# Performance work log

Hardware: AMD Instinct MI355X
Metric: run time of the kernel (lower is better)

## Reference

```python
import jax, jax.numpy as jnp
import numpy as np

B, N, C = 8, 16384, 256

def setup_inputs() -> dict:
    key = jax.random.key(0)
    ks = jax.random.split(key, 5)
    scale = 1.0 / np.sqrt(C)
    return {
        "x_in": jax.random.normal(ks[0], (B, N, C), dtype=jnp.float32),
        "Wq": jax.random.normal(ks[1], (C, C), dtype=jnp.float32) * scale,
        "bq": jax.random.normal(ks[2], (C,), dtype=jnp.float32) * scale,
        "Wk": jax.random.normal(ks[3], (C, C), dtype=jnp.float32) * scale,
        "bk": jax.random.normal(ks[4], (C,), dtype=jnp.float32) * scale,
    }

def reference(x_in, Wq, bq, Wk, bk):
    b, n, c = x_in.shape
    # Faithful to torch: reshape (NOT transpose) to [B, C, N]
    x = x_in.reshape(b, c, n)
    # 1x1 Conv1d == per-position linear over channel dim
    Q = jnp.einsum('oc,bcn->bon', Wq, x) + bq[None, :, None]  # [B,C,N]
    K = jnp.einsum('oc,bcn->bon', Wk, x) + bk[None, :, None]  # [B,C,N]
    # Q @ K^T over length axis -> channel-channel scores [B,C,C]
    scores = jnp.einsum('bcn,bdn->bcd', Q, K)
    c_c = jax.nn.softmax(scores, axis=-1)
    # x_in @ c_c + residual -> [B,N,C]
    return jnp.einsum('bnc,bcd->bnd', x_in, c_c) + x_in
```

## Files before the change

### kernel.cpp

```cpp
#include <hip/hip_runtime.h>

#define Bn 8
#define Nn 16384
#define Cn 256
#define NC 32

typedef __attribute__((ext_vector_type(4)))  float f32x4;
typedef __attribute__((ext_vector_type(16))) float f32x16;
typedef __attribute__((ext_vector_type(8)))  _Float16 f16x8;
typedef __attribute__((ext_vector_type(8)))  unsigned short u16x8;

static __device__ __forceinline__ unsigned short f2h(float f) {
    return __builtin_bit_cast(unsigned short, (_Float16)f);
}
static __device__ __forceinline__ f32x16 mfma16h(u16x8 a, u16x8 b, f32x16 c) {
    return __builtin_amdgcn_mfma_f32_32x32x16_f16(
        __builtin_bit_cast(f16x8, a), __builtin_bit_cast(f16x8, b), c, 0, 0, 0);
}

__global__ __launch_bounds__(256, 2) void k_gram(
    const float* __restrict__ x, float* __restrict__ gpart,
    float* __restrict__ spart) {
  const int b    = blockIdx.x & 7;
  const int loc  = blockIdx.x >> 3;
  const int ck   = loc >> 1;
  const int half = loc & 1;

  __shared__ __align__(16) char smem[2][32768];

  const int t     = threadIdx.x;
  const int lane  = t & 63;
  const int w     = t >> 6;
  const int ln    = lane & 31, kh = lane >> 5;
  const int rquad = t >> 4;
  const int c4    = t & 15;

  const float* xb = x + (size_t)b * ((size_t)Cn * Nn) + (size_t)ck * 512;

  f32x16 acc[4][2];
#pragma unroll
  for (int m = 0; m < 4; ++m)
#pragma unroll
    for (int n = 0; n < 2; ++n)
#pragma unroll
      for (int i = 0; i < 16; ++i) acc[m][n][i] = 0.f;

  float srow[16];
#pragma unroll
  for (int p = 0; p < 16; ++p) srow[p] = 0.f;

  f32x4 ldA[8], ldB[8];
#define LOADA(s) { _Pragma("unroll") for (int p = 0; p < 8; ++p) \
    ldA[p] = *(const f32x4*)(xb + (size_t)(p * 16 + rquad) * Nn + (s) * 64 + c4 * 4); }
#define LOADB(s) { _Pragma("unroll") for (int p = 0; p < 8; ++p) \
    ldB[p] = *(const f32x4*)(xb + (size_t)((p + 8) * 16 + rquad) * Nn + (s) * 64 + c4 * 4); }

  LOADA(0); LOADB(0);

  for (int s = 0; s < 8; ++s) {
    char* buf = smem[s & 1];
    __syncthreads();
#pragma unroll
    for (int p = 0; p < 8; ++p) {
      f32x4 v = ldA[p];
      srow[p] += (v.x + v.y) + (v.z + v.w);
      int r = p * 16 + rquad;
      ushort4 hv = make_ushort4(f2h(v.x), f2h(v.y), f2h(v.z), f2h(v.w));
      *(ushort4*)(buf + r * 128 + ((((c4 >> 1) + r) & 7) << 4) + (c4 & 1) * 8) = hv;
    }
#pragma unroll
    for (int p = 0; p < 8; ++p) {
      f32x4 v = ldB[p];
      srow[p + 8] += (v.x + v.y) + (v.z + v.w);
      int r = (p + 8) * 16 + rquad;
      ushort4 hv = make_ushort4(f2h(v.x), f2h(v.y), f2h(v.z), f2h(v.w));
      *(ushort4*)(buf + r * 128 + ((((c4 >> 1) + r) & 7) << 4) + (c4 & 1) * 8) = hv;
    }
    __syncthreads();
    if (s < 7) { LOADA(s + 1); LOADB(s + 1); }
#pragma unroll
    for (int ks = 0; ks < 4; ++ks) {
      const int cp = ks * 2 + kh;
      u16x8 A[4], Bv[2];
#pragma unroll
      for (int m = 0; m < 4; ++m) {
        int r = half * 128 + m * 32 + ln;
        A[m] = *(const u16x8*)(buf + r * 128 + (((cp + r) & 7) << 4));
      }
#pragma unroll
      for (int n = 0; n < 2; ++n) {
        int r = w * 64 + n * 32 + ln;
        Bv[n] = *(const u16x8*)(buf + r * 128 + (((cp + r) & 7) << 4));
      }
#pragma unroll
      for (int m = 0; m < 4; ++m)
#pragma unroll
        for (int n = 0; n < 2; ++n)
          acc[m][n] = mfma16h(A[m], Bv[n], acc[m][n]);
    }
  }
#undef LOADA
#undef LOADB

  if (half == 0) {
#pragma unroll
    for (int p = 0; p < 16; ++p) {
      float v = srow[p];
      v += __shfl_xor(v, 1);
      v += __shfl_xor(v, 2);
      v += __shfl_xor(v, 4);
      v += __shfl_xor(v, 8);
      if (c4 == 0) spart[(size_t)(b * NC + ck) * Cn + p * 16 + rquad] = v;
    }
  }

  float* gp = gpart + (size_t)(b * NC + ck) * (Cn * Cn);
#pragma unroll
  for (int m = 0; m < 4; ++m)
#pragma unroll
    for (int n = 0; n < 2; ++n)
#pragma unroll
      for (int r2 = 0; r2 < 16; ++r2) {
        int row = half * 128 + m * 32 + (r2 & 3) + 8 * (r2 >> 2) + 4 * kh;
        int col = w * 64 + n * 32 + ln;
        gp[row * Cn + col] = acc[m][n][r2];
      }
}

__global__ __launch_bounds__(256) void k_misc(
    const float* __restrict__ spart, const float* __restrict__ wk,
    const float* __restrict__ bk, float* __restrict__ sv,
    float* __restrict__ wkT, float* __restrict__ kN) {
  const int bb = blockIdx.x, t = threadIdx.x;
  __shared__ float s_l[256];
  float a = 0.f;
#pragma unroll
  for (int q = 0; q < NC; ++q) a += spart[(size_t)(bb * NC + q) * Cn + t];
  sv[bb * Cn + t] = a;
  s_l[t] = a;
#pragma unroll
  for (int j = 0; j < 32; ++j) {
    int k = bb * 32 + j;
    wkT[k * Cn + t] = wk[t * Cn + k];
  }
  __syncthreads();
  float k2 = 0.f;
  for (int c = 0; c < 256; ++c) k2 += wk[t * Cn + c] * s_l[c];
  kN[bb * Cn + t] = k2 + 16384.f * bk[t];
}

__global__ __launch_bounds__(256) void k_gk(
    const float* __restrict__ gpart, const float* __restrict__ sv,
    const float* __restrict__ wkT, const float* __restrict__ bk,
    float* __restrict__ GK) {
  const int b = blockIdx.x >> 6, tile = blockIdx.x & 63;
  const int r0 = tile * 4, t = threadIdx.x;
  __shared__ float g_l[4][256];

  float a[4] = {0.f, 0.f, 0.f, 0.f};
  const float* gp = gpart + (size_t)b * NC * 65536 + r0 * 256 + t;
  for (int ck = 0; ck < NC; ++ck) {
#pragma unroll
    for (int j = 0; j < 4; ++j) a[j] += gp[(size_t)ck * 65536 + j * 256];
  }
#pragma unroll
  for (int j = 0; j < 4; ++j) g_l[j][t] = a[j];
  __syncthreads();

  float acc[4] = {0.f, 0.f, 0.f, 0.f};
  for (int k0 = 0; k0 < 256; k0 += 4) {
    float w0 = wkT[(k0 + 0) * 256 + t];
    float w1 = wkT[(k0 + 1) * 256 + t];
    float w2 = wkT[(k0 + 2) * 256 + t];
    float w3 = wkT[(k0 + 3) * 256 + t];
#pragma unroll
    for (int r = 0; r < 4; ++r) {
      f32x4 gv = *(const f32x4*)(&g_l[r][k0]);
      acc[r] += gv.x * w0 + gv.y * w1 + gv.z * w2 + gv.w * w3;
    }
  }
  float bkt = bk[t];
#pragma unroll
  for (int r = 0; r < 4; ++r) {
    float svr = sv[b * 256 + r0 + r];
    GK[((size_t)b * 256 + r0 + r) * 256 + t] = acc[r] + svr * bkt;
  }
}

__global__ __launch_bounds__(256) void k_scores(
    const float* __restrict__ wq, const float* __restrict__ GK,
    const float* __restrict__ bq, const float* __restrict__ kN,
    unsigned short* __restrict__ ccB) {
  const int b    = blockIdx.x >> 5;
  const int tile = blockIdx.x & 31;
  const int c0   = tile * 8;
  const int t    = threadIdx.x;

  __shared__ float wq_l[8][256];
  __shared__ float sc_l[8][256];
  __shared__ unsigned short cct_l[256][8];

#pragma unroll
  for (int j = 0; j < 8; ++j) wq_l[j][t] = wq[(c0 + j) * Cn + t];
  __syncthreads();

  float acc[8];
#pragma unroll
  for (int r = 0; r < 8; ++r) acc[r] = 0.f;
  for (int k0 = 0; k0 < 256; k0 += 4) {
    float g0 = GK[((size_t)b * 256 + k0 + 0) * 256 + t];
    float g1 = GK[((size_t)b * 256 + k0 + 1) * 256 + t];
    float g2 = GK[((size_t)b * 256 + k0 + 2) * 256 + t];
    float g3 = GK[((size_t)b * 256 + k0 + 3) * 256 + t];
#pragma unroll
    for (int r = 0; r < 8; ++r) {
      f32x4 qv = *(const f32x4*)(&wq_l[r][k0]);
      acc[r] += qv.x * g0 + qv.y * g1 + qv.z * g2 + qv.w * g3;
    }
  }
  float kNt = kN[b * 256 + t];
#pragma unroll
  for (int r = 0; r < 8; ++r) sc_l[r][t] = acc[r] + bq[c0 + r] * kNt;
  __syncthreads();

  const int r = t >> 5, sub = t & 31;
  float v[8];
#pragma unroll
  for (int j = 0; j < 8; ++j) v[j] = sc_l[r][sub + 32 * j];
  float mx = v[0];
#pragma unroll
  for (int j = 1; j < 8; ++j) mx = fmaxf(mx, v[j]);
#pragma unroll
  for (int msk = 16; msk >= 1; msk >>= 1) mx = fmaxf(mx, __shfl_xor(mx, msk, 32));
  float se = 0.f;
#pragma unroll
  for (int j = 0; j < 8; ++j) { v[j] = __expf(v[j] - mx); se += v[j]; }
#pragma unroll
  for (int msk = 16; msk >= 1; msk >>= 1) se += __shfl_xor(se, msk, 32);
  float inv = 1.f / se;
#pragma unroll
  for (int j = 0; j < 8; ++j) {
    int d = sub + 32 * j;
    float cc = v[j] * inv + ((d == c0 + r) ? 1.f : 0.f);
    cct_l[d][r] = f2h(cc);
  }
  __syncthreads();
  *(uint4*)(ccB + (size_t)b * 65536 + (size_t)(tile * 256 + t) * 8) =
      *(const uint4*)(&cct_l[t][0]);
}

__global__ __launch_bounds__(256, 2) void k_out(
    const float* __restrict__ x, const unsigned short* __restrict__ ccB,
    float* __restrict__ out) {
  const int b  = blockIdx.x & 7;
  const int n0 = (blockIdx.x >> 3) << 7;
  const float* xb = x + (size_t)b * ((size_t)Nn * Cn) + (size_t)n0 * Cn;
  const unsigned short* cb = ccB + (size_t)b * 65536;
  float* ob = out + (size_t)b * ((size_t)Nn * Cn) + (size_t)n0 * Cn;

  __shared__ __align__(16) char smem[65536];

  const int t    = threadIdx.x;
  const int lane = t & 63;
  const int w    = t >> 6;
  const int ln = lane & 31;
  const int kh = lane >> 5;

  f32x16 acc[4][2];
#pragma unroll
  for (int m = 0; m < 4; ++m)
#pragma unroll
    for (int n = 0; n < 2; ++n)
#pragma unroll
      for (int i = 0; i < 16; ++i) acc[m][n][i] = 0.f;

#pragma unroll
  for (int q = 0; q < 4; ++q) {
    f32x4 v[8];
#pragma unroll
    for (int i = 0; i < 8; ++i)
      v[i] = *(const f32x4*)(xb + (size_t)((q * 8 + i) * 256 + t) * 4);
#pragma unroll
    for (int i = 0; i < 8; ++i) {
      int fi = (q * 8 + i) * 256 + t;
      int r = fi >> 6, c4 = fi & 63;
      ushort4 hv = make_ushort4(f2h(v[i].x), f2h(v[i].y), f2h(v[i].z), f2h(v[i].w));
      *(ushort4*)(smem + r * 512 + ((((c4 >> 1) + r) & 31) << 4) + (c4 & 1) * 8) = hv;
    }
  }
  __syncthreads();

#pragma unroll
  for (int ks = 0; ks < 16; ++ks) {
    const int cp = ks * 2 + kh;
    u16x8 A[4], Bv[2];
#pragma unroll
    for (int m = 0; m < 4; ++m) {
      int r = m * 32 + ln;
      A[m] = *(const u16x8*)(smem + r * 512 + (((cp + r) & 31) << 4));
    }
#pragma unroll
    for (int n = 0; n < 2; ++n) {
      int d = w * 64 + n * 32 + ln;
      Bv[n] = *(const u16x8*)(cb + (size_t)cp * 2048 + (size_t)d * 8);
    }
#pragma unroll
    for (int m = 0; m < 4; ++m)
#pragma unroll
      for (int n = 0; n < 2; ++n)
        acc[m][n] = mfma16h(A[m], Bv[n], acc[m][n]);
  }

#pragma unroll
  for (int m = 0; m < 4; ++m)
#pragma unroll
    for (int n = 0; n < 2; ++n)
#pragma unroll
      for (int r2 = 0; r2 < 16; ++r2) {
        int row = m * 32 + (r2 & 3) + 8 * (r2 >> 2) + 4 * kh;
        int col = w * 64 + n * 32 + ln;
        ob[(size_t)row * Cn + col] = acc[m][n][r2];
      }
}

extern "C" void kernel_launch(void* const* d_in, const int* in_sizes, int n_in,
                              void* d_out, int out_size, void* d_ws, size_t ws_size,
                              hipStream_t stream) {
  const float* x  = (const float*)d_in[0];
  const float* wq = (const float*)d_in[1];
  const float* bq = (const float*)d_in[2];
  const float* wk = (const float*)d_in[3];
  const float* bk = (const float*)d_in[4];
  float* out = (float*)d_out;

  float* gpart = (float*)d_ws;
  float* spart = gpart + (size_t)Bn * NC * 65536;
  float* sv    = spart + (size_t)Bn * NC * 256;
  float* wkT   = sv + (size_t)Bn * 256;
  float* kN    = wkT + 65536;
  float* GK    = kN + (size_t)Bn * 256;
  unsigned short* ccB = (unsigned short*)(GK + (size_t)Bn * 65536);

  hipLaunchKernelGGL(k_gram,   dim3(Bn * NC * 2), dim3(256), 0, stream, x, gpart, spart);
  hipLaunchKernelGGL(k_misc,   dim3(Bn),          dim3(256), 0, stream, spart, wk, bk, sv, wkT, kN);
  hipLaunchKernelGGL(k_gk,     dim3(Bn * 64),     dim3(256), 0, stream, gpart, sv, wkT, bk, GK);
  hipLaunchKernelGGL(k_scores, dim3(Bn * 32),     dim3(256), 0, stream, wq, GK, bq, kN, ccB);
  hipLaunchKernelGGL(k_out,    dim3(Bn * 128),    dim3(256), 0, stream, x, ccB, out);
}
```

Measured before the change: 135.1 us.

## Merge gram half-blocks into one 512-thread block and drop Wk transpose

The gram kernel now uses one 512-thread block per (batch, chunk) instead of two 256-thread blocks that each loaded the full 256-row x tile. Each wave pair splits the 256x256 output by row half and column quarter, so every x element is read from global memory and converted to fp16 only once. Separately, the Wk transpose in k_misc is removed and k_gk reads Wk rows directly with vector loads. That saves a scattered transpose write, but k_gk's per-thread row reads are strided across threads and coalesce poorly. The larger block may also lower occupancy given the register-heavy accumulators.

```diff
diff --git a/kernel.cpp b/kernel.cpp
--- a/kernel.cpp
+++ b/kernel.cpp
@@ -18,19 +18,19 @@
         __builtin_bit_cast(f16x8, a), __builtin_bit_cast(f16x8, b), c, 0, 0, 0);
 }
 
-__global__ __launch_bounds__(256, 2) void k_gram(
+__global__ __launch_bounds__(512, 2) void k_gram(
     const float* __restrict__ x, float* __restrict__ gpart,
     float* __restrict__ spart) {
-  const int b    = blockIdx.x & 7;
-  const int loc  = blockIdx.x >> 3;
-  const int ck   = loc >> 1;
-  const int half = loc & 1;
+  const int b  = blockIdx.x & 7;
+  const int ck = blockIdx.x >> 3;
 
   __shared__ __align__(16) char smem[2][32768];
 
   const int t     = threadIdx.x;
   const int lane  = t & 63;
   const int w     = t >> 6;
+  const int wm    = w & 1;
+  const int wn    = w >> 1;
   const int ln    = lane & 31, kh = lane >> 5;
   const int rquad = t >> 4;
   const int c4    = t & 15;
@@ -45,51 +45,41 @@
 #pragma unroll
       for (int i = 0; i < 16; ++i) acc[m][n][i] = 0.f;
 
-  float srow[16];
-#pragma unroll
-  for (int p = 0; p < 16; ++p) srow[p] = 0.f;
-
-  f32x4 ldA[8], ldB[8];
-#define LOADA(s) { _Pragma("unroll") for (int p = 0; p < 8; ++p) \
-    ldA[p] = *(const f32x4*)(xb + (size_t)(p * 16 + rquad) * Nn + (s) * 64 + c4 * 4); }
-#define LOADB(s) { _Pragma("unroll") for (int p = 0; p < 8; ++p) \
-    ldB[p] = *(const f32x4*)(xb + (size_t)((p + 8) * 16 + rquad) * Nn + (s) * 64 + c4 * 4); }
-
-  LOADA(0); LOADB(0);
+  float srow[8];
+#pragma unroll
+  for (int p = 0; p < 8; ++p) srow[p] = 0.f;
+
+  f32x4 ld[8];
+#define LOADS(s) { _Pragma("unroll") for (int p = 0; p < 8; ++p) \
+    ld[p] = *(const f32x4*)(xb + (size_t)(p * 32 + rquad) * Nn + (s) * 64 + c4 * 4); }
+
+  LOADS(0);
 
   for (int s = 0; s < 8; ++s) {
     char* buf = smem[s & 1];
     __syncthreads();
 #pragma unroll
     for (int p = 0; p < 8; ++p) {
-      f32x4 v = ldA[p];
+      f32x4 v = ld[p];
       srow[p] += (v.x + v.y) + (v.z + v.w);
-      int r = p * 16 + rquad;
+      int r = p * 32 + rquad;
       ushort4 hv = make_ushort4(f2h(v.x), f2h(v.y), f2h(v.z), f2h(v.w));
       *(ushort4*)(buf + r * 128 + ((((c4 >> 1) + r) & 7) << 4) + (c4 & 1) * 8) = hv;
     }
-#pragma unroll
-    for (int p = 0; p < 8; ++p) {
-      f32x4 v = ldB[p];
-      srow[p + 8] += (v.x + v.y) + (v.z + v.w);
-      int r = (p + 8) * 16 + rquad;
-      ushort4 hv = make_ushort4(f2h(v.x), f2h(v.y), f2h(v.z), f2h(v.w));
-      *(ushort4*)(buf + r * 128 + ((((c4 >> 1) + r) & 7) << 4) + (c4 & 1) * 8) = hv;
-    }
     __syncthreads();
-    if (s < 7) { LOADA(s + 1); LOADB(s + 1); }
+    if (s < 7) LOADS(s + 1);
 #pragma unroll
     for (int ks = 0; ks < 4; ++ks) {
       const int cp = ks * 2 + kh;
       u16x8 A[4], Bv[2];
 #pragma unroll
       for (int m = 0; m < 4; ++m) {
-        int r = half * 128 + m * 32 + ln;
+        int r = wm * 128 + m * 32 + ln;
         A[m] = *(const u16x8*)(buf + r * 128 + (((cp + r) & 7) << 4));
       }
 #pragma unroll
       for (int n = 0; n < 2; ++n) {
-        int r = w * 64 + n * 32 + ln;
+        int r = wn * 64 + n * 32 + ln;
         Bv[n] = *(const u16x8*)(buf + r * 128 + (((cp + r) & 7) << 4));
       }
 #pragma unroll
@@ -99,19 +89,16 @@
           acc[m][n] = mfma16h(A[m], Bv[n], acc[m][n]);
     }
   }
-#undef LOADA
-#undef LOADB
-
-  if (half == 0) {
-#pragma unroll
-    for (int p = 0; p < 16; ++p) {
-      float v = srow[p];
-      v += __shfl_xor(v, 1);
-      v += __shfl_xor(v, 2);
-      v += __shfl_xor(v, 4);
-      v += __shfl_xor(v, 8);
-      if (c4 == 0) spart[(size_t)(b * NC + ck) * Cn + p * 16 + rquad] = v;
-    }
+#undef LOADS
+
+#pragma unroll
+  for (int p = 0; p < 8; ++p) {
+    float v = srow[p];
+    v += __shfl_xor(v, 1);
+    v += __shfl_xor(v, 2);
+    v += __shfl_xor(v, 4);
+    v += __shfl_xor(v, 8);
+    if (c4 == 0) spart[(size_t)(b * NC + ck) * Cn + p * 32 + rquad] = v;
   }
 
   float* gp = gpart + (size_t)(b * NC + ck) * (Cn * Cn);
@@ -121,8 +108,8 @@
     for (int n = 0; n < 2; ++n)
 #pragma unroll
       for (int r2 = 0; r2 < 16; ++r2) {
-        int row = half * 128 + m * 32 + (r2 & 3) + 8 * (r2 >> 2) + 4 * kh;
-        int col = w * 64 + n * 32 + ln;
+        int row = wm * 128 + m * 32 + (r2 & 3) + 8 * (r2 >> 2) + 4 * kh;
+        int col = wn * 64 + n * 32 + ln;
         gp[row * Cn + col] = acc[m][n][r2];
       }
 }
@@ -130,7 +117,7 @@
 __global__ __launch_bounds__(256) void k_misc(
     const float* __restrict__ spart, const float* __restrict__ wk,
     const float* __restrict__ bk, float* __restrict__ sv,
-    float* __restrict__ wkT, float* __restrict__ kN) {
+    float* __restrict__ kN) {
   const int bb = blockIdx.x, t = threadIdx.x;
   __shared__ float s_l[256];
   float a = 0.f;
@@ -138,20 +125,19 @@
   for (int q = 0; q < NC; ++q) a += spart[(size_t)(bb * NC + q) * Cn + t];
   sv[bb * Cn + t] = a;
   s_l[t] = a;
-#pragma unroll
-  for (int j = 0; j < 32; ++j) {
-    int k = bb * 32 + j;
-    wkT[k * Cn + t] = wk[t * Cn + k];
-  }
   __syncthreads();
   float k2 = 0.f;
-  for (int c = 0; c < 256; ++c) k2 += wk[t * Cn + c] * s_l[c];
+  for (int c0 = 0; c0 < 256; c0 += 4) {
+    f32x4 wv = *(const f32x4*)(&wk[t * Cn + c0]);
+    f32x4 sl = *(const f32x4*)(&s_l[c0]);
+    k2 += wv.x * sl.x + wv.y * sl.y + wv.z * sl.z + wv.w * sl.w;
+  }
   kN[bb * Cn + t] = k2 + 16384.f * bk[t];
 }
 
 __global__ __launch_bounds__(256) void k_gk(
     const float* __restrict__ gpart, const float* __restrict__ sv,
-    const float* __restrict__ wkT, const float* __restrict__ bk,
+    const float* __restrict__ wk, const float* __restrict__ bk,
     float* __restrict__ GK) {
   const int b = blockIdx.x >> 6, tile = blockIdx.x & 63;
   const int r0 = tile * 4, t = threadIdx.x;
@@ -169,14 +155,11 @@
 
   float acc[4] = {0.f, 0.f, 0.f, 0.f};
   for (int k0 = 0; k0 < 256; k0 += 4) {
-    float w0 = wkT[(k0 + 0) * 256 + t];
-    float w1 = wkT[(k0 + 1) * 256 + t];
-    float w2 = wkT[(k0 + 2) * 256 + t];
-    float w3 = wkT[(k0 + 3) * 256 + t];
+    f32x4 wv = *(const f32x4*)(&wk[t * Cn + k0]);
 #pragma unroll
     for (int r = 0; r < 4; ++r) {
       f32x4 gv = *(const f32x4*)(&g_l[r][k0]);
-      acc[r] += gv.x * w0 + gv.y * w1 + gv.z * w2 + gv.w * w3;
+      acc[r] += gv.x * wv.x + gv.y * wv.y + gv.z * wv.z + gv.w * wv.w;
     }
   }
   float bkt = bk[t];
@@ -336,14 +319,13 @@
   float* gpart = (float*)d_ws;
   float* spart = gpart + (size_t)Bn * NC * 65536;
   float* sv    = spart + (size_t)Bn * NC * 256;
-  float* wkT   = sv + (size_t)Bn * 256;
-  float* kN    = wkT + 65536;
+  float* kN    = sv + (size_t)Bn * 256;
   float* GK    = kN + (size_t)Bn * 256;
   unsigned short* ccB = (unsigned short*)(GK + (size_t)Bn * 65536);
 
-  hipLaunchKernelGGL(k_gram,   dim3(Bn * NC * 2), dim3(256), 0, stream, x, gpart, spart);
-  hipLaunchKernelGGL(k_misc,   dim3(Bn),          dim3(256), 0, stream, spart, wk, bk, sv, wkT, kN);
-  hipLaunchKernelGGL(k_gk,     dim3(Bn * 64),     dim3(256), 0, stream, gpart, sv, wkT, bk, GK);
-  hipLaunchKernelGGL(k_scores, dim3(Bn * 32),     dim3(256), 0, stream, wq, GK, bq, kN, ccB);
-  hipLaunchKernelGGL(k_out,    dim3(Bn * 128),    dim3(256), 0, stream, x, ccB, out);
-}
+  hipLaunchKernelGGL(k_gram,   dim3(Bn * NC),  dim3(512), 0, stream, x, gpart, spart);
+  hipLaunchKernelGGL(k_misc,   dim3(Bn),       dim3(256), 0, stream, spart, wk, bk, sv, kN);
+  hipLaunchKernelGGL(k_gk,     dim3(Bn * 64),  dim3(256), 0, stream, gpart, sv, wk, bk, GK);
+  hipLaunchKernelGGL(k_scores, dim3(Bn * 32),  dim3(256), 0, stream, wq, GK, bq, kN, ccB);
+  hipLaunchKernelGGL(k_out,    dim3(Bn * 128), dim3(256), 0, stream, x, ccB, out);
+}
```

Result: slower. 147.1 us (+8.9%).

## Reduce Gram partials with global atomics instead of a partial buffer

Applied to the files above, without the earlier changes.

k_gram now atomically adds its 256x256 partial Gram tile and its row sums directly into per-batch accumulators, zeroed by a memset, instead of writing 32 partial copies per batch that k_gk and k_misc later sum. The wkT transpose is removed, and k_gk and k_misc read Wk rows with vector loads instead. This avoids writing and re-reading about 64 MB of partials. In exchange it issues many float atomics that contend on the same addresses, adds a memset launch, and makes the summation order nondeterministic.

```diff
diff --git a/kernel.cpp b/kernel.cpp
--- a/kernel.cpp
+++ b/kernel.cpp
@@ -19,8 +19,8 @@
 }
 
 __global__ __launch_bounds__(256, 2) void k_gram(
-    const float* __restrict__ x, float* __restrict__ gpart,
-    float* __restrict__ spart) {
+    const float* __restrict__ x, float* __restrict__ G,
+    float* __restrict__ sv) {
   const int b    = blockIdx.x & 7;
   const int loc  = blockIdx.x >> 3;
   const int ck   = loc >> 1;
@@ -110,11 +110,11 @@
       v += __shfl_xor(v, 2);
       v += __shfl_xor(v, 4);
       v += __shfl_xor(v, 8);
-      if (c4 == 0) spart[(size_t)(b * NC + ck) * Cn + p * 16 + rquad] = v;
-    }
-  }
-
-  float* gp = gpart + (size_t)(b * NC + ck) * (Cn * Cn);
+      if (c4 == 0) atomicAdd(&sv[b * Cn + p * 16 + rquad], v);
+    }
+  }
+
+  float* gb = G + (size_t)b * 65536;
 #pragma unroll
   for (int m = 0; m < 4; ++m)
 #pragma unroll
@@ -123,60 +123,46 @@
       for (int r2 = 0; r2 < 16; ++r2) {
         int row = half * 128 + m * 32 + (r2 & 3) + 8 * (r2 >> 2) + 4 * kh;
         int col = w * 64 + n * 32 + ln;
-        gp[row * Cn + col] = acc[m][n][r2];
+        atomicAdd(&gb[row * Cn + col], acc[m][n][r2]);
       }
 }
 
 __global__ __launch_bounds__(256) void k_misc(
-    const float* __restrict__ spart, const float* __restrict__ wk,
-    const float* __restrict__ bk, float* __restrict__ sv,
-    float* __restrict__ wkT, float* __restrict__ kN) {
+    const float* __restrict__ sv, const float* __restrict__ wk,
+    const float* __restrict__ bk, float* __restrict__ kN) {
   const int bb = blockIdx.x, t = threadIdx.x;
   __shared__ float s_l[256];
-  float a = 0.f;
-#pragma unroll
-  for (int q = 0; q < NC; ++q) a += spart[(size_t)(bb * NC + q) * Cn + t];
-  sv[bb * Cn + t] = a;
-  s_l[t] = a;
-#pragma unroll
-  for (int j = 0; j < 32; ++j) {
-    int k = bb * 32 + j;
-    wkT[k * Cn + t] = wk[t * Cn + k];
-  }
+  s_l[t] = sv[bb * Cn + t];
   __syncthreads();
   float k2 = 0.f;
-  for (int c = 0; c < 256; ++c) k2 += wk[t * Cn + c] * s_l[c];
+  for (int c0 = 0; c0 < 256; c0 += 4) {
+    f32x4 wv = *(const f32x4*)(&wk[t * Cn + c0]);
+    f32x4 sl = *(const f32x4*)(&s_l[c0]);
+    k2 += wv.x * sl.x + wv.y * sl.y + wv.z * sl.z + wv.w * sl.w;
+  }
   kN[bb * Cn + t] = k2 + 16384.f * bk[t];
 }
 
 __global__ __launch_bounds__(256) void k_gk(
-    const float* __restrict__ gpart, const float* __restrict__ sv,
-    const float* __restrict__ wkT, const float* __restrict__ bk,
+    const float* __restrict__ G, const float* __restrict__ sv,
+    const float* __restrict__ wk, const float* __restrict__ bk,
     float* __restrict__ GK) {
   const int b = blockIdx.x >> 6, tile = blockIdx.x & 63;
   const int r0 = tile * 4, t = threadIdx.x;
   __shared__ float g_l[4][256];
 
-  float a[4] = {0.f, 0.f, 0.f, 0.f};
-  const float* gp = gpart + (size_t)b * NC * 65536 + r0 * 256 + t;
-  for (int ck = 0; ck < NC; ++ck) {
-#pragma unroll
-    for (int j = 0; j < 4; ++j) a[j] += gp[(size_t)ck * 65536 + j * 256];
-  }
-#pragma unroll
-  for (int j = 0; j < 4; ++j) g_l[j][t] = a[j];
+#pragma unroll
+  for (int j = 0; j < 4; ++j)
+    g_l[j][t] = G[(size_t)b * 65536 + (r0 + j) * 256 + t];
   __syncthreads();
 
   float acc[4] = {0.f, 0.f, 0.f, 0.f};
   for (int k0 = 0; k0 < 256; k0 += 4) {
-    float w0 = wkT[(k0 + 0) * 256 + t];
-    float w1 = wkT[(k0 + 1) * 256 + t];
-    float w2 = wkT[(k0 + 2) * 256 + t];
-    float w3 = wkT[(k0 + 3) * 256 + t];
+    f32x4 wv = *(const f32x4*)(&wk[t * Cn + k0]);
 #pragma unroll
     for (int r = 0; r < 4; ++r) {
       f32x4 gv = *(const f32x4*)(&g_l[r][k0]);
-      acc[r] += gv.x * w0 + gv.y * w1 + gv.z * w2 + gv.w * w3;
+      acc[r] += gv.x * wv.x + gv.y * wv.y + gv.z * wv.z + gv.w * wv.w;
     }
   }
   float bkt = bk[t];
@@ -333,17 +319,16 @@
   const float* bk = (const float*)d_in[4];
   float* out = (float*)d_out;
 
-  float* gpart = (float*)d_ws;
-  float* spart = gpart + (size_t)Bn * NC * 65536;
-  float* sv    = spart + (size_t)Bn * NC * 256;
-  float* wkT   = sv + (size_t)Bn * 256;
-  float* kN    = wkT + 65536;
-  float* GK    = kN + (size_t)Bn * 256;
+  float* G   = (float*)d_ws;
+  float* sv  = G + (size_t)Bn * 65536;
+  float* kN  = sv + (size_t)Bn * 256;
+  float* GK  = kN + (size_t)Bn * 256;
   unsigned short* ccB = (unsigned short*)(GK + (size_t)Bn * 65536);
 
-  hipLaunchKernelGGL(k_gram,   dim3(Bn * NC * 2), dim3(256), 0, stream, x, gpart, spart);
-  hipLaunchKernelGGL(k_misc,   dim3(Bn),          dim3(256), 0, stream, spart, wk, bk, sv, wkT, kN);
-  hipLaunchKernelGGL(k_gk,     dim3(Bn * 64),     dim3(256), 0, stream, gpart, sv, wkT, bk, GK);
+  hipMemsetAsync(G, 0, ((size_t)Bn * 65536 + (size_t)Bn * 256) * sizeof(float), stream);
+  hipLaunchKernelGGL(k_gram,   dim3(Bn * NC * 2), dim3(256), 0, stream, x, G, sv);
+  hipLaunchKernelGGL(k_misc,   dim3(Bn),          dim3(256), 0, stream, sv, wk, bk, kN);
+  hipLaunchKernelGGL(k_gk,     dim3(Bn * 64),     dim3(256), 0, stream, G, sv, wk, bk, GK);
   hipLaunchKernelGGL(k_scores, dim3(Bn * 32),     dim3(256), 0, stream, wq, GK, bq, kN, ccB);
   hipLaunchKernelGGL(k_out,    dim3(Bn * 128),    dim3(256), 0, stream, x, ccB, out);
 }
```

Result: slower. 175.3 us (+29.8%).

## Store partial Gram matrices in fp16 and drop Wk transpose

Applied to the files above, without the earlier changes.

The per-chunk partial Gram matrices written by k_gram are stored as fp16 instead of fp32, halving the write and re-read traffic of the roughly 64 MB partial buffer. k_gk now reads these with 8-wide vector loads, handles 8 rows per block instead of 4, and reads Wk rows directly with vector loads, so k_misc no longer builds a transposed Wk. The cost is lower precision in the partial sums, which feed the softmax scores and could introduce error. The Wk reads in k_gk are now strided by row across threads and therefore less coalesced.

```diff
diff --git a/kernel.cpp b/kernel.cpp
--- a/kernel.cpp
+++ b/kernel.cpp
@@ -13,13 +13,16 @@
 static __device__ __forceinline__ unsigned short f2h(float f) {
     return __builtin_bit_cast(unsigned short, (_Float16)f);
 }
+static __device__ __forceinline__ float h2f(unsigned short h) {
+    return (float)__builtin_bit_cast(_Float16, h);
+}
 static __device__ __forceinline__ f32x16 mfma16h(u16x8 a, u16x8 b, f32x16 c) {
     return __builtin_amdgcn_mfma_f32_32x32x16_f16(
         __builtin_bit_cast(f16x8, a), __builtin_bit_cast(f16x8, b), c, 0, 0, 0);
 }
 
 __global__ __launch_bounds__(256, 2) void k_gram(
-    const float* __restrict__ x, float* __restrict__ gpart,
+    const float* __restrict__ x, unsigned short* __restrict__ gph,
     float* __restrict__ spart) {
   const int b    = blockIdx.x & 7;
   const int loc  = blockIdx.x >> 3;
@@ -114,7 +117,7 @@
     }
   }
 
-  float* gp = gpart + (size_t)(b * NC + ck) * (Cn * Cn);
+  unsigned short* gp = gph + (size_t)(b * NC + ck) * (Cn * Cn);
 #pragma unroll
   for (int m = 0; m < 4; ++m)
 #pragma unroll
@@ -123,14 +126,14 @@
       for (int r2 = 0; r2 < 16; ++r2) {
         int row = half * 128 + m * 32 + (r2 & 3) + 8 * (r2 >> 2) + 4 * kh;
         int col = w * 64 + n * 32 + ln;
-        gp[row * Cn + col] = acc[m][n][r2];
+        gp[row * Cn + col] = f2h(acc[m][n][r2]);
       }
 }
 
 __global__ __launch_bounds__(256) void k_misc(
     const float* __restrict__ spart, const float* __restrict__ wk,
     const float* __restrict__ bk, float* __restrict__ sv,
-    float* __restrict__ wkT, float* __restrict__ kN) {
+    float* __restrict__ kN) {
   const int bb = blockIdx.x, t = threadIdx.x;
   __shared__ float s_l[256];
   float a = 0.f;
@@ -138,50 +141,53 @@
   for (int q = 0; q < NC; ++q) a += spart[(size_t)(bb * NC + q) * Cn + t];
   sv[bb * Cn + t] = a;
   s_l[t] = a;
-#pragma unroll
-  for (int j = 0; j < 32; ++j) {
-    int k = bb * 32 + j;
-    wkT[k * Cn + t] = wk[t * Cn + k];
-  }
   __syncthreads();
   float k2 = 0.f;
-  for (int c = 0; c < 256; ++c) k2 += wk[t * Cn + c] * s_l[c];
+  for (int c0 = 0; c0 < 256; c0 += 4) {
+    f32x4 wv = *(const f32x4*)(&wk[t * Cn + c0]);
+    f32x4 sl = *(const f32x4*)(&s_l[c0]);
+    k2 += wv.x * sl.x + wv.y * sl.y + wv.z * sl.z + wv.w * sl.w;
+  }
   kN[bb * Cn + t] = k2 + 16384.f * bk[t];
 }
 
 __global__ __launch_bounds__(256) void k_gk(
-    const float* __restrict__ gpart, const float* __restrict__ sv,
-    const float* __restrict__ wkT, const float* __restrict__ bk,
+    const unsigned short* __restrict__ gph, const float* __restrict__ sv,
+    const float* __restrict__ wk, const float* __restrict__ bk,
     float* __restrict__ GK) {
-  const int b = blockIdx.x >> 6, tile = blockIdx.x & 63;
-  const int r0 = tile * 4, t = threadIdx.x;
-  __shared__ float g_l[4][256];
-
-  float a[4] = {0.f, 0.f, 0.f, 0.f};
-  const float* gp = gpart + (size_t)b * NC * 65536 + r0 * 256 + t;
+  const int b = blockIdx.x >> 5, tile = blockIdx.x & 31;
+  const int r0 = tile * 8, t = threadIdx.x;
+  __shared__ float g_l[8][256];
+
+  const int j  = t >> 5;
+  const int c8 = t & 31;
+  float a8[8];
+#pragma unroll
+  for (int i = 0; i < 8; ++i) a8[i] = 0.f;
+  const unsigned short* gp = gph + (size_t)b * NC * 65536 + (r0 + j) * 256 + c8 * 8;
   for (int ck = 0; ck < NC; ++ck) {
-#pragma unroll
-    for (int j = 0; j < 4; ++j) a[j] += gp[(size_t)ck * 65536 + j * 256];
-  }
-#pragma unroll
-  for (int j = 0; j < 4; ++j) g_l[j][t] = a[j];
-  __syncthreads();
-
-  float acc[4] = {0.f, 0.f, 0.f, 0.f};
+    u16x8 v = *(const u16x8*)(gp + (size_t)ck * 65536);
+#pragma unroll
+    for (int i = 0; i < 8; ++i) a8[i] += h2f(v[i]);
+  }
+#pragma unroll
+  for (int i = 0; i < 8; ++i) g_l[j][c8 * 8 + i] = a8[i];
+  __syncthreads();
+
+  float acc[8];
+#pragma unroll
+  for (int r = 0; r < 8; ++r) acc[r] = 0.f;
   for (int k0 = 0; k0 < 256; k0 += 4) {
-    float w0 = wkT[(k0 + 0) * 256 + t];
-    float w1 = wkT[(k0 + 1) * 256 + t];
-    float w2 = wkT[(k0 + 2) * 256 + t];
-    float w3 = wkT[(k0 + 3) * 256 + t];
-#pragma unroll
-    for (int r = 0; r < 4; ++r) {
+    f32x4 wv = *(const f32x4*)(&wk[t * Cn + k0]);
+#pragma unroll
+    for (int r = 0; r < 8; ++r) {
       f32x4 gv = *(const f32x4*)(&g_l[r][k0]);
-      acc[r] += gv.x * w0 + gv.y * w1 + gv.z * w2 + gv.w * w3;
+      acc[r] += gv.x * wv.x + gv.y * wv.y + gv.z * wv.z + gv.w * wv.w;
     }
   }
   float bkt = bk[t];
 #pragma unroll
-  for (int r = 0; r < 4; ++r) {
+  for (int r = 0; r < 8; ++r) {
     float svr = sv[b * 256 + r0 + r];
     GK[((size_t)b * 256 + r0 + r) * 256 + t] = acc[r] + svr * bkt;
   }
@@ -333,17 +339,16 @@
   const float* bk = (const float*)d_in[4];
   float* out = (float*)d_out;
 
-  float* gpart = (float*)d_ws;
-  float* spart = gpart + (size_t)Bn * NC * 65536;
+  unsigned short* gph = (unsigned short*)d_ws;
+  float* spart = (float*)(gph + (size_t)Bn * NC * 65536);
   float* sv    = spart + (size_t)Bn * NC * 256;
-  float* wkT   = sv + (size_t)Bn * 256;
-  float* kN    = wkT + 65536;
+  float* kN    = sv + (size_t)Bn * 256;
   float* GK    = kN + (size_t)Bn * 256;
   unsigned short* ccB = (unsigned short*)(GK + (size_t)Bn * 65536);
 
-  hipLaunchKernelGGL(k_gram,   dim3(Bn * NC * 2), dim3(256), 0, stream, x, gpart, spart);
-  hipLaunchKernelGGL(k_misc,   dim3(Bn),          dim3(256), 0, stream, spart, wk, bk, sv, wkT, kN);
-  hipLaunchKernelGGL(k_gk,     dim3(Bn * 64),     dim3(256), 0, stream, gpart, sv, wkT, bk, GK);
+  hipLaunchKernelGGL(k_gram,   dim3(Bn * NC * 2), dim3(256), 0, stream, x, gph, spart);
+  hipLaunchKernelGGL(k_misc,   dim3(Bn),          dim3(256), 0, stream, spart, wk, bk, sv, kN);
+  hipLaunchKernelGGL(k_gk,     dim3(Bn * 32),     dim3(256), 0, stream, gph, sv, wk, bk, GK);
   hipLaunchKernelGGL(k_scores, dim3(Bn * 32),     dim3(256), 0, stream, wq, GK, bq, kN, ccB);
   hipLaunchKernelGGL(k_out,    dim3(Bn * 128),    dim3(256), 0, stream, x, ccB, out);
 }
```

Result: no change. 137.7 us (+1.9%).
